# Performance work log

Hardware: AMD Instinct MI355X
Metric: run time of the kernel (lower is better)

## Reference

```python
import jax, jax.numpy as jnp
import numpy as np

S, B, D, H = 1024, 8, 768, 12
PROMPT_NUM = 8
DH = D // H


def setup_inputs() -> dict:
    key = jax.random.key(0)
    ks = jax.random.split(key, 5)
    scale = 1.0 / np.sqrt(D)
    return {
        "x": jax.random.normal(ks[0], (S, B, D), dtype=jnp.float32),
        "in_proj_weight": jax.random.normal(ks[1], (3 * D, D), dtype=jnp.float32) * scale,
        "in_proj_bias": jax.random.normal(ks[2], (3 * D,), dtype=jnp.float32) * 0.02,
        "out_w": jax.random.normal(ks[3], (D, D), dtype=jnp.float32) * scale,
        "out_b": jax.random.normal(ks[4], (D,), dtype=jnp.float32) * 0.02,
    }


def reference(x, in_proj_weight, in_proj_bias, out_w, out_b):
    # x: (S, B, D) -> (B, S, D)
    xt = jnp.transpose(x, (1, 0, 2))
    qkv = xt @ in_proj_weight.T + in_proj_bias  # (B, S, 3D)
    q, k, v = jnp.split(qkv, 3, axis=-1)
    q = q.reshape(B, S, H, DH)
    k = k.reshape(B, S, H, DH)
    v = v.reshape(B, S, H, DH)
    # affinity (n, q, k, h); scale by sqrt(head_dim)
    aff = jnp.einsum("nqhc,nkhc->nqkh", q / np.sqrt(DH), k)
    # prompt masking: CLS_MASK | PROMPT_MASK
    tokens = S - PROMPT_NUM
    m = np.zeros((S, S), dtype=bool)
    m[0, tokens:] = True          # CLS_MASK: CLS query can't attend to prompts
    m[tokens:, tokens:] = True    # PROMPT_MASK: prompts can't attend to prompts
    m = jnp.asarray(m)
    aff = jnp.where(m[None, :, :, None], jnp.float32(-10000.0), aff)
    # softmax over key axis (dim=-2 of nqkh)
    aff = jax.nn.softmax(aff, axis=2)
    mix = jnp.einsum("nqlh,nlhc->nqhc", aff, v)  # (B, S, H, DH)
    out = mix.reshape(B, S, D) @ out_w.T + out_b
    # transpose back to (S, B, ...)
    return (
        jnp.transpose(q, (1, 0, 2, 3)),
        jnp.transpose(k, (1, 0, 2, 3)),
        jnp.transpose(v, (1, 0, 2, 3)),
        jnp.transpose(out, (1, 0, 2)),
    )
```

## Files before the change

kernel.cpp:

```cpp
#include <hip/hip_runtime.h>
#include <hip/hip_bf16.h>


typedef unsigned short u16;
typedef __attribute__((ext_vector_type(8))) short short8;
typedef __attribute__((ext_vector_type(4))) short short4v;
typedef __attribute__((ext_vector_type(4))) float floatx4;
typedef __attribute__((ext_vector_type(16))) float floatx16;
typedef __attribute__((ext_vector_type(4))) unsigned short ushort4v;
typedef __attribute__((ext_vector_type(2))) unsigned int uint2v;

#define NB 8
#define NS 1024
#define NH 12
#define ND 768
#define DHD 64
#define TOKENS 1016
#define QKV_OUT_STRIDE 6291456

#if __has_builtin(__builtin_amdgcn_exp2f)
#define EXP2(x) __builtin_amdgcn_exp2f(x)
#else
#define EXP2(x) exp2f(x)
#endif

#if defined(__HIP_DEVICE_COMPILE__)
  #if __has_builtin(__builtin_amdgcn_mfma_f32_16x16x16bf16_1k)
    #define MFMA16(a, b, c) __builtin_amdgcn_mfma_f32_16x16x16bf16_1k(a, b, c, 0, 0, 0)
  #else
    #define MFMA16(a, b, c) __builtin_amdgcn_mfma_f32_16x16x16_bf16(a, b, c, 0, 0, 0)
  #endif
  #define GLD16(g, l)                                                        \
    __builtin_amdgcn_global_load_lds(                                        \
        (const __attribute__((address_space(1))) void*)(g),                  \
        (__attribute__((address_space(3))) void*)(l), 16, 0, 0)
  #define SETPRIO(n) __builtin_amdgcn_s_setprio(n)
#else
  #define MFMA16(a, b, c) (c)
  #define GLD16(g, l) ((void)0)
  #define SETPRIO(n) ((void)0)
#endif

__device__ __forceinline__ u16 f2bf(float f) {
  union { float f; unsigned u; } c; c.f = f;
  return (u16)((c.u + 0x7fffu + ((c.u >> 16) & 1u)) >> 16);
}

#define CVT_B0 6144
#define CVT_B1 1728
#define CVT_B2 576
__global__ __launch_bounds__(256) void cvt3(
    const float* __restrict__ s0, u16* __restrict__ d0,
    const float* __restrict__ s1, u16* __restrict__ d1,
    const float* __restrict__ s2, u16* __restrict__ d2) {
  int blk = blockIdx.x;
  if (blk < CVT_B0) {
    const int i = (blk * 256 + (int)threadIdx.x) * 4;
    const float4 v = *(const float4*)(s0 + i);
    const int sb = i / ND;
    const int dd = i - sb * ND;
    const int m = ((sb & 7) << 10) | (sb >> 3);
    ushort4v o;
    o.x = f2bf(v.x); o.y = f2bf(v.y); o.z = f2bf(v.z); o.w = f2bf(v.w);
    *(ushort4v*)(d0 + m * ND + dd) = o;
    return;
  }
  const float* s; u16* d;
  if (blk < CVT_B0 + CVT_B1) { s = s1; d = d1; blk -= CVT_B0; }
  else { s = s2; d = d2; blk -= CVT_B0 + CVT_B1; }
  const int i = (blk * 256 + (int)threadIdx.x) * 4;
  const float4 v = *(const float4*)(s + i);
  ushort4v o;
  o.x = f2bf(v.x); o.y = f2bf(v.y); o.z = f2bf(v.z); o.w = f2bf(v.w);
  *(ushort4v*)(d + i) = o;
}

#define GEMM_STAGE(buf, k0)                                                  \
  do {                                                                       \
    GLD16(ga0 + (k0), &buf##A[c0 * 16][0]);                                  \
    GLD16(ga1 + (k0), &buf##A[c0 * 16 + 16][0]);                             \
    GLD16(gb0 + (k0), &buf##B[c0 * 16][0]);                                  \
    GLD16(gb1 + (k0), &buf##B[c0 * 16 + 16][0]);                             \
  } while (0)

#define GEMM_COMPUTE(buf)                                                    \
  do {                                                                       \
    short8 af[2][2], bfr[2][2];                                              \
    _Pragma("unroll")                                                        \
    for (int mt = 0; mt < 2; ++mt)                                           \
      _Pragma("unroll")                                                      \
      for (int ks = 0; ks < 2; ++ks)                                         \
        af[mt][ks] =                                                         \
            *(const short8*)&buf##A[wm * 64 + mt * 32 + l31][ks * 16 + hi8]; \
    _Pragma("unroll")                                                        \
    for (int nt = 0; nt < 2; ++nt)                                           \
      _Pragma("unroll")                                                      \
      for (int ks = 0; ks < 2; ++ks)                                         \
        bfr[nt][ks] =                                                        \
            *(const short8*)&buf##B[wn * 64 + nt * 32 + l31][ks * 16 + hi8]; \
    _Pragma("unroll")                                                        \
    for (int mt = 0; mt < 2; ++mt)                                           \
      _Pragma("unroll")                                                      \
      for (int nt = 0; nt < 2; ++nt)                                         \
        _Pragma("unroll")                                                    \
        for (int ks = 0; ks < 2; ++ks)                                       \
          acc[mt][nt] = __builtin_amdgcn_mfma_f32_32x32x16_bf16(             \
              af[mt][ks], bfr[nt][ks], acc[mt][nt], 0, 0, 0);                \
  } while (0)

__global__ __launch_bounds__(256) void qkv_gemm(
    const u16* __restrict__ Xb, const u16* __restrict__ Wb,
    const float* __restrict__ bias, float* __restrict__ out,
    u16* __restrict__ Kb) {
  __shared__ __align__(16) u16 p0A[128][32];
  __shared__ __align__(16) u16 p0B[128][32];
  __shared__ __align__(16) u16 p1A[128][32];
  __shared__ __align__(16) u16 p1B[128][32];
  const int tid = threadIdx.x;
  const int lane = tid & 63, wave = tid >> 6;
  const int l31 = lane & 31, hi8 = (lane >> 5) * 8;
  const int wm = wave & 1, wn = wave >> 1;
  const int L = (int)blockIdx.x + 64 * (int)blockIdx.y;
  const int xcd = L & 7, i = L >> 3;
  const int mblk = (xcd + 8 * (i & 7)) * 128;
  const int nblk = (i >> 3) * 128;

  floatx16 acc[2][2];
#pragma unroll
  for (int i2 = 0; i2 < 2; ++i2)
#pragma unroll
    for (int j = 0; j < 2; ++j) acc[i2][j] = (floatx16)0.f;

  const int lr = lane >> 2;
  const int lc = (lane & 3) * 8;
  const int c0 = wave * 2;
  const int r0 = c0 * 16 + lr, r1 = r0 + 16;
  const u16* ga0 = Xb + (mblk + r0) * ND + lc;
  const u16* ga1 = Xb + (mblk + r1) * ND + lc;
  const u16* gb0 = Wb + (nblk + r0) * ND + lc;
  const u16* gb1 = Wb + (nblk + r1) * ND + lc;

  GEMM_STAGE(p0, 0);
  __syncthreads();
  for (int kt = 0; kt < 24; kt += 2) {
    GEMM_STAGE(p1, (kt + 1) * 32);
    GEMM_COMPUTE(p0);
    __syncthreads();
    if (kt + 2 < 24) GEMM_STAGE(p0, (kt + 2) * 32);
    GEMM_COMPUTE(p1);
    __syncthreads();
  }

  const int seg = nblk / ND;
  const int nbase = nblk - seg * ND;
  float* outp = out + seg * QKV_OUT_STRIDE;
#pragma unroll
  for (int mt = 0; mt < 2; ++mt) {
#pragma unroll
    for (int nt = 0; nt < 2; ++nt) {
#pragma unroll
      for (int r = 0; r < 16; ++r) {
        const int grow = (r & 3) + 8 * (r >> 2) + (hi8 >> 1);
        const int gm = mblk + wm * 64 + mt * 32 + grow;
        const int b = gm >> 10, s = gm & 1023;
        const int gn = nblk + wn * 64 + nt * 32 + l31;
        const int nn = nbase + wn * 64 + nt * 32 + l31;
        const float val = acc[mt][nt][r] + bias[gn];
        outp[(s * NB + b) * ND + nn] = val;
        if (seg == 1) {
          Kb[(((size_t)b * NH + (nn >> 6)) * NS + s) * DHD + (nn & 63)] =
              f2bf(val);
        }
      }
    }
  }
}

__global__ __launch_bounds__(256) void prep(
    const float* __restrict__ V, u16* __restrict__ Vt) {
  __shared__ u16 tile[DHD][40];
  const int t = threadIdx.x;
  const int bh = blockIdx.y;
  const int b = bh / NH, h = bh % NH;
  const int s0 = blockIdx.x * 32;
  const int sl = t >> 3;
  const int c0 = (t & 7) * 8;
  const int s = s0 + sl;
  const float* src = V + ((s * NB + b) * NH + h) * DHD + c0;
  const float4 v0 = *(const float4*)src;
  const float4 v1 = *(const float4*)(src + 4);
  tile[c0 + 0][sl] = f2bf(v0.x); tile[c0 + 1][sl] = f2bf(v0.y);
  tile[c0 + 2][sl] = f2bf(v0.z); tile[c0 + 3][sl] = f2bf(v0.w);
  tile[c0 + 4][sl] = f2bf(v1.x); tile[c0 + 5][sl] = f2bf(v1.y);
  tile[c0 + 6][sl] = f2bf(v1.z); tile[c0 + 7][sl] = f2bf(v1.w);
  __syncthreads();
  const int c = t >> 2;
  const int so = (t & 3) * 8;
  *(short8*)(Vt + ((size_t)bh * DHD + c) * NS + s0 + so) =
      *(const short8*)&tile[c][so];
}

__global__ __launch_bounds__(256) void attn(
    const float* __restrict__ Q, const u16* __restrict__ Kb,
    const u16* __restrict__ Vt, u16* __restrict__ mix) {
  __shared__ __align__(16) u16 Kt[128][72];
  __shared__ __align__(16) u16 Vs[64][136];
  const int tid = threadIdx.x;
  const int lane = tid & 63, wave = tid >> 6;
  const int l15 = lane & 15, quad = lane >> 4;
  const int L = (int)blockIdx.x + 8 * (int)blockIdx.y;
  const int xcd = L & 7, tt = L >> 3;
  const int bh = xcd + 8 * (tt >> 3);
  const int qx = tt & 7;
  const int b = bh / NH, h = bh % NH;
  const int qb = qx * 128 + wave * 32;

  const float SC = 0.125f * 1.44269504089f;

  short8 qf[2][2];
  bool qmask[2];
#pragma unroll
  for (int j = 0; j < 2; ++j) {
    const int qj = qb + j * 16 + l15;
    qmask[j] = (qj == 0 || qj >= TOKENS);
    const float* qp = Q + ((qj * NB + b) * NH + h) * DHD + quad * 8;
#pragma unroll
    for (int e = 0; e < 8; ++e) {
      qf[j][0][e] = (short)f2bf(qp[e] * SC);
      qf[j][1][e] = (short)f2bf(qp[32 + e] * SC);
    }
  }

  floatx4 O[2][4];
#pragma unroll
  for (int j = 0; j < 2; ++j)
#pragma unroll
    for (int g = 0; g < 4; ++g) O[j][g] = (floatx4)0.f;
  floatx4 liacc[2];
  liacc[0] = (floatx4)0.f;
  liacc[1] = (floatx4)0.f;
  short4v ones4;
#pragma unroll
  for (int e = 0; e < 4; ++e) ones4[e] = (short)0x3F80;

  const u16* kg = Kb + (size_t)bh * NS * DHD;
  const u16* vg = Vt + (size_t)bh * DHD * NS;

  const int krow = tid >> 1;
  const int kcol = (tid & 1) * 32;
  const int vrow = tid >> 2;
  const int vcol = (tid & 3) * 32;

  short8 pk[4], pv[4];
#pragma unroll
  for (int u = 0; u < 4; ++u) {
    pk[u] = *(const short8*)(kg + krow * DHD + kcol + u * 8);
    pv[u] = *(const short8*)(vg + vrow * NS + vcol + u * 8);
  }

  for (int it = 0; it < 8; ++it) {
#pragma unroll
    for (int u = 0; u < 4; ++u) {
      *(short8*)&Kt[krow][kcol + u * 8] = pk[u];
      *(short8*)&Vs[vrow][vcol + u * 8] = pv[u];
    }
    __syncthreads();
    if (it < 7) {
      const int k0 = (it + 1) * 128;
#pragma unroll
      for (int u = 0; u < 4; ++u) {
        pk[u] = *(const short8*)(kg + (k0 + krow) * DHD + kcol + u * 8);
        pv[u] = *(const short8*)(vg + vrow * NS + k0 + vcol + u * 8);
      }
    }
#pragma unroll
    for (int half = 0; half < 2; ++half) {
      const bool mrow = (it == 7) && (half == 1) && (quad >= 2);
#pragma unroll
      for (int sub = 0; sub < 4; ++sub) {
        const int kr = half * 64 + sub * 16 + l15;
        const short8 kf0 = *(const short8*)&Kt[kr][quad * 8];
        const short8 kf1 = *(const short8*)&Kt[kr][32 + quad * 8];
        short4v pb[2];
#pragma unroll
        for (int j = 0; j < 2; ++j) {
          floatx4 a = (floatx4)0.f;
          a = __builtin_amdgcn_mfma_f32_16x16x32_bf16(kf0, qf[j][0], a, 0, 0, 0);
          a = __builtin_amdgcn_mfma_f32_16x16x32_bf16(kf1, qf[j][1], a, 0, 0, 0);
          float p[4];
#pragma unroll
          for (int r = 0; r < 4; ++r) p[r] = EXP2(a[r]);
          if (sub == 3 && mrow && qmask[j]) {
#pragma unroll
            for (int r = 0; r < 4; ++r) p[r] = 0.f;
          }
          __hip_bfloat162 w0 = __float22bfloat162_rn(make_float2(p[0], p[1]));
          __hip_bfloat162 w1 = __float22bfloat162_rn(make_float2(p[2], p[3]));
          uint2v pw;
          pw.x = *(const unsigned*)&w0;
          pw.y = *(const unsigned*)&w1;
          pb[j] = __builtin_bit_cast(short4v, pw);
        }
        SETPRIO(1);
#pragma unroll
        for (int g = 0; g < 4; ++g) {
          const short4v vf =
              *(const short4v*)&Vs[g * 16 + l15][half * 64 + sub * 16 + quad * 4];
          O[0][g] = MFMA16(vf, pb[0], O[0][g]);
          O[1][g] = MFMA16(vf, pb[1], O[1][g]);
        }
        liacc[0] = MFMA16(ones4, pb[0], liacc[0]);
        liacc[1] = MFMA16(ones4, pb[1], liacc[1]);
        SETPRIO(0);
      }
    }
    __syncthreads();
  }

#pragma unroll
  for (int j = 0; j < 2; ++j) {
    const float rl = 1.0f / liacc[j][0];
    const int qj = qb + j * 16 + l15;
    u16* mp = mix + ((size_t)b * NS + qj) * ND + h * DHD + quad * 4;
#pragma unroll
    for (int g = 0; g < 4; ++g) {
      ushort4v o;
#pragma unroll
      for (int r = 0; r < 4; ++r) o[r] = f2bf(O[j][g][r] * rl);
      *(ushort4v*)(mp + g * 16) = o;
    }
  }
}

__global__ __launch_bounds__(256) void out_gemm(
    const u16* __restrict__ A, const u16* __restrict__ Wb,
    const float* __restrict__ bias, float* __restrict__ out) {
  __shared__ __align__(16) u16 p0A[128][32];
  __shared__ __align__(16) u16 p0B[128][32];
  __shared__ __align__(16) u16 p1A[128][32];
  __shared__ __align__(16) u16 p1B[128][32];
  const int tid = threadIdx.x;
  const int lane = tid & 63, wave = tid >> 6;
  const int l31 = lane & 31, hi8 = (lane >> 5) * 8;
  const int wm = wave & 1, wn = wave >> 1;
  const int L = (int)blockIdx.x + 64 * (int)blockIdx.y;
  const int xcd = L & 7, i = L >> 3;
  const int mblk = (xcd + 8 * (i & 7)) * 128;
  const int nblk = (i >> 3) * 128;

  floatx16 acc[2][2];
#pragma unroll
  for (int i2 = 0; i2 < 2; ++i2)
#pragma unroll
    for (int j = 0; j < 2; ++j) acc[i2][j] = (floatx16)0.f;

  const int lr = lane >> 2;
  const int lc = (lane & 3) * 8;
  const int c0 = wave * 2;
  const int r0 = c0 * 16 + lr, r1 = r0 + 16;
  const u16* ga0 = A + (mblk + r0) * ND + lc;
  const u16* ga1 = A + (mblk + r1) * ND + lc;
  const u16* gb0 = Wb + (nblk + r0) * ND + lc;
  const u16* gb1 = Wb + (nblk + r1) * ND + lc;

  GEMM_STAGE(p0, 0);
  __syncthreads();
  for (int kt = 0; kt < 24; kt += 2) {
    GEMM_STAGE(p1, (kt + 1) * 32);
    GEMM_COMPUTE(p0);
    __syncthreads();
    if (kt + 2 < 24) GEMM_STAGE(p0, (kt + 2) * 32);
    GEMM_COMPUTE(p1);
    __syncthreads();
  }

#pragma unroll
  for (int mt = 0; mt < 2; ++mt) {
#pragma unroll
    for (int nt = 0; nt < 2; ++nt) {
#pragma unroll
      for (int r = 0; r < 16; ++r) {
        const int grow = (r & 3) + 8 * (r >> 2) + (hi8 >> 1);
        const int gm = mblk + wm * 64 + mt * 32 + grow;
        const int b = gm >> 10, s = gm & 1023;
        const int gn = nblk + wn * 64 + nt * 32 + l31;
        out[(s * NB + b) * ND + gn] = acc[mt][nt][r] + bias[gn];
      }
    }
  }
}

extern "C" void kernel_launch(void* const* d_in, const int* in_sizes, int n_in,
                              void* d_out, int out_size, void* d_ws, size_t ws_size,
                              hipStream_t stream) {
  const float* X  = (const float*)d_in[0];
  const float* W  = (const float*)d_in[1];
  const float* Bi = (const float*)d_in[2];
  const float* Ow = (const float*)d_in[3];
  const float* Ob = (const float*)d_in[4];
  float* out = (float*)d_out;

  u16* Xb  = (u16*)d_ws;
  u16* Wb  = Xb  + 6291456;
  u16* Owb = Wb  + 1769472;
  u16* Vt  = Owb + 589824;
  u16* Kb  = Vt  + 6291456;
  u16* mix = Kb  + 6291456;

  cvt3<<<CVT_B0 + CVT_B1 + CVT_B2, 256, 0, stream>>>(X, Xb, W, Wb, Ow, Owb);
  qkv_gemm<<<dim3(64, 18), 256, 0, stream>>>(Xb, Wb, Bi, out, Kb);
  prep<<<dim3(32, 96), 256, 0, stream>>>(out + 2 * QKV_OUT_STRIDE, Vt);
  attn<<<dim3(8, 96), 256, 0, stream>>>(out, Kb, Vt, mix);
  out_gemm<<<dim3(64, 6), 256, 0, stream>>>(mix, Owb, Ob, out + 3 * QKV_OUT_STRIDE);
}
```

Before: 235.6 us.

## Split attention over two key halves and merge partials in a combine kernel

The attention grid gains a z dimension so each block handles half of the keys (512), which doubles the number of blocks from 768 to 1536. Each half writes a normalized bf16 partial output plus its softmax denominator, reusing the Xb and Wb workspace regions. A new combine kernel merges the halves by denominator weights. Softmax runs without a running max, so exp-sum weighting is exact. The cost is an extra kernel launch, extra global traffic for the partials, and a second bf16 rounding of the intermediate output.

```diff
diff --git a/kernel.cpp b/kernel.cpp
--- a/kernel.cpp
+++ b/kernel.cpp
@@ -17,6 +17,7 @@
 #define DHD 64
 #define TOKENS 1016
 #define QKV_OUT_STRIDE 6291456
+#define LI_STRIDE 98304
 
 #if __has_builtin(__builtin_amdgcn_exp2f)
 #define EXP2(x) __builtin_amdgcn_exp2f(x)
@@ -44,6 +45,10 @@
 __device__ __forceinline__ u16 f2bf(float f) {
   union { float f; unsigned u; } c; c.f = f;
   return (u16)((c.u + 0x7fffu + ((c.u >> 16) & 1u)) >> 16);
+}
+__device__ __forceinline__ float bf2f(u16 v) {
+  union { unsigned u; float f; } c; c.u = ((unsigned)v) << 16;
+  return c.f;
 }
 
 #define CVT_B0 6144
@@ -202,7 +207,8 @@
 
 __global__ __launch_bounds__(256) void attn(
     const float* __restrict__ Q, const u16* __restrict__ Kb,
-    const u16* __restrict__ Vt, u16* __restrict__ mix) {
+    const u16* __restrict__ Vt, u16* __restrict__ mix,
+    u16* __restrict__ mixB, float* __restrict__ liw) {
   __shared__ __align__(16) u16 Kt[128][72];
   __shared__ __align__(16) u16 Vs[64][136];
   const int tid = threadIdx.x;
@@ -212,6 +218,8 @@
   const int xcd = L & 7, tt = L >> 3;
   const int bh = xcd + 8 * (tt >> 3);
   const int qx = tt & 7;
+  const int z = (int)blockIdx.z;
+  const int kbase = z * 512;
   const int b = bh / NH, h = bh % NH;
   const int qb = qx * 128 + wave * 32;
 
@@ -254,19 +262,19 @@
   short8 pk[4], pv[4];
 #pragma unroll
   for (int u = 0; u < 4; ++u) {
-    pk[u] = *(const short8*)(kg + krow * DHD + kcol + u * 8);
-    pv[u] = *(const short8*)(vg + vrow * NS + vcol + u * 8);
-  }
-
-  for (int it = 0; it < 8; ++it) {
+    pk[u] = *(const short8*)(kg + (kbase + krow) * DHD + kcol + u * 8);
+    pv[u] = *(const short8*)(vg + vrow * NS + kbase + vcol + u * 8);
+  }
+
+  for (int it = 0; it < 4; ++it) {
 #pragma unroll
     for (int u = 0; u < 4; ++u) {
       *(short8*)&Kt[krow][kcol + u * 8] = pk[u];
       *(short8*)&Vs[vrow][vcol + u * 8] = pv[u];
     }
     __syncthreads();
-    if (it < 7) {
-      const int k0 = (it + 1) * 128;
+    if (it < 3) {
+      const int k0 = kbase + (it + 1) * 128;
 #pragma unroll
       for (int u = 0; u < 4; ++u) {
         pk[u] = *(const short8*)(kg + (k0 + krow) * DHD + kcol + u * 8);
@@ -275,7 +283,7 @@
     }
 #pragma unroll
     for (int half = 0; half < 2; ++half) {
-      const bool mrow = (it == 7) && (half == 1) && (quad >= 2);
+      const bool mrow = (z == 1) && (it == 3) && (half == 1) && (quad >= 2);
 #pragma unroll
       for (int sub = 0; sub < 4; ++sub) {
         const int kr = half * 64 + sub * 16 + l15;
@@ -317,11 +325,15 @@
     __syncthreads();
   }
 
+  u16* dst = z ? mixB : mix;
+  float* lw = liw + z * LI_STRIDE;
 #pragma unroll
   for (int j = 0; j < 2; ++j) {
-    const float rl = 1.0f / liacc[j][0];
+    const float l = liacc[j][0];
+    const float rl = 1.0f / l;
     const int qj = qb + j * 16 + l15;
-    u16* mp = mix + ((size_t)b * NS + qj) * ND + h * DHD + quad * 4;
+    if (quad == 0) lw[(b * NS + qj) * NH + h] = l;
+    u16* mp = dst + ((size_t)b * NS + qj) * ND + h * DHD + quad * 4;
 #pragma unroll
     for (int g = 0; g < 4; ++g) {
       ushort4v o;
@@ -330,6 +342,25 @@
       *(ushort4v*)(mp + g * 16) = o;
     }
   }
+}
+
+__global__ __launch_bounds__(256) void combine(
+    u16* __restrict__ A0, const u16* __restrict__ A1,
+    const float* __restrict__ liw) {
+  const int i = ((int)blockIdx.x * 256 + (int)threadIdx.x) * 4;
+  const int row = i / ND;
+  const int h = (i - row * ND) >> 6;
+  const float l0 = liw[row * NH + h];
+  const float l1 = liw[LI_STRIDE + row * NH + h];
+  const float inv = 1.0f / (l0 + l1);
+  const float w0 = l0 * inv, w1 = l1 * inv;
+  const ushort4v a0 = *(const ushort4v*)(A0 + i);
+  const ushort4v a1 = *(const ushort4v*)(A1 + i);
+  ushort4v o;
+#pragma unroll
+  for (int r = 0; r < 4; ++r)
+    o[r] = f2bf(bf2f(a0[r]) * w0 + bf2f(a1[r]) * w1);
+  *(ushort4v*)(A0 + i) = o;
 }
 
 __global__ __launch_bounds__(256) void out_gemm(
@@ -406,10 +437,12 @@
   u16* Vt  = Owb + 589824;
   u16* Kb  = Vt  + 6291456;
   u16* mix = Kb  + 6291456;
+  float* liw = (float*)Wb;
 
   cvt3<<<CVT_B0 + CVT_B1 + CVT_B2, 256, 0, stream>>>(X, Xb, W, Wb, Ow, Owb);
   qkv_gemm<<<dim3(64, 18), 256, 0, stream>>>(Xb, Wb, Bi, out, Kb);
   prep<<<dim3(32, 96), 256, 0, stream>>>(out + 2 * QKV_OUT_STRIDE, Vt);
-  attn<<<dim3(8, 96), 256, 0, stream>>>(out, Kb, Vt, mix);
+  attn<<<dim3(8, 96, 2), 256, 0, stream>>>(out, Kb, Vt, mix, Xb, liw);
+  combine<<<6144, 256, 0, stream>>>(mix, Xb, liw);
   out_gemm<<<dim3(64, 6), 256, 0, stream>>>(mix, Owb, Ob, out + 3 * QKV_OUT_STRIDE);
 }
```

Result: slower. 243.2 us (+3.3%).
